# Kernel optimization log

Measured on AMD Instinct MI355X. Metric: run time of the kernel, lower is better.

Reference implementation:

```python
import jax, jax.numpy as jnp
import numpy as np

B, N, C = 4, 2048, 768
H = 12
DH = C // H
HID = 4 * C
EPS = 1e-5


def layer_norm(x, g, b):
    mu = jnp.mean(x, axis=-1, keepdims=True)
    var = jnp.mean(jnp.square(x - mu), axis=-1, keepdims=True)
    return (x - mu) * jax.lax.rsqrt(var + EPS) * g + b


def setup_inputs() -> dict:
    key = jax.random.key(0)
    ks = jax.random.split(key, 8)
    s = 0.02
    return {
        "x": jax.random.normal(ks[0], (B, N, C), dtype=jnp.float32),
        "ln1_g": jnp.ones((C,), jnp.float32),
        "ln1_b": jnp.zeros((C,), jnp.float32),
        # weights stored [in, out] (transpose of torch Linear.weight)
        "w_qkv": jax.random.normal(ks[1], (C, 3 * C), jnp.float32) * s,
        "w_proj": jax.random.normal(ks[2], (C, C), jnp.float32) * s,
        "b_proj": jnp.zeros((C,), jnp.float32),
        "ln2_g": jnp.ones((C,), jnp.float32),
        "ln2_b": jnp.zeros((C,), jnp.float32),
        "w1": jax.random.normal(ks[3], (C, HID), jnp.float32) * s,
        "b1": jnp.zeros((HID,), jnp.float32),
        "w2": jax.random.normal(ks[4], (HID, C), jnp.float32) * s,
        "b2": jnp.zeros((C,), jnp.float32),
    }


def reference(x, ln1_g, ln1_b, w_qkv, w_proj, b_proj, ln2_g, ln2_b, w1, b1, w2, b2):
    # --- attention sub-block (qkv_bias=False, eval mode: dropout/droppath = identity) ---
    h = layer_norm(x, ln1_g, ln1_b)
    qkv = (h @ w_qkv).reshape(B, N, 3, H, DH)          # [B,N,3,H,Dh]
    q, k, v = (qkv[:, :, i].transpose(0, 2, 1, 3) for i in range(3))  # [B,H,N,Dh]
    scale = DH ** -0.5
    attn = jax.nn.softmax(jnp.einsum("bhnd,bhmd->bhnm", q, k) * scale, axis=-1)
    o = jnp.einsum("bhnm,bhmd->bhnd", attn, v).transpose(0, 2, 1, 3).reshape(B, N, C)
    x = x + (o @ w_proj + b_proj)
    # --- MLP sub-block (exact GELU, matching torch nn.GELU) ---
    h2 = layer_norm(x, ln2_g, ln2_b)
    m = jax.nn.gelu(h2 @ w1 + b1, approximate=False) @ w2 + b2
    return x + m
```

## Files before the change

kernel.cpp:

```cpp
#include <hip/hip_runtime.h>
#include <hip/hip_bf16.h>

#define B_ 4
#define N_ 2048
#define C_ 768
#define H_ 12
#define DH_ 64
#define HID_ 3072
#define ROWS_ (B_*N_)

typedef short short8 __attribute__((ext_vector_type(8)));
typedef float f32x4 __attribute__((ext_vector_type(4)));

static __device__ __forceinline__ unsigned short f2bf(float f) {
    __hip_bfloat16 h = __float2bfloat16(f);
    unsigned short u;
    __builtin_memcpy(&u, &h, 2);
    return u;
}

static __device__ __forceinline__ void gload16(const unsigned short* g, unsigned short* l) {
    __builtin_amdgcn_global_load_lds(
        (const __attribute__((address_space(1))) unsigned int*)g,
        (__attribute__((address_space(3))) unsigned int*)l, 16, 0, 0);
}

__global__ __launch_bounds__(256, 4) void ln_kernel(
    const float* __restrict__ x, const float* __restrict__ g,
    const float* __restrict__ bta, unsigned short* __restrict__ out) {
    int row = blockIdx.x;
    const float* xr = x + (size_t)row * C_;
    int t = threadIdx.x;
    float v0 = xr[t], v1 = xr[t + 256], v2 = xr[t + 512];
    float s = v0 + v1 + v2, ss = v0*v0 + v1*v1 + v2*v2;
    #pragma unroll
    for (int o = 32; o > 0; o >>= 1) { s += __shfl_down(s, o); ss += __shfl_down(ss, o); }
    __shared__ float red[10];
    int wid = t >> 6;
    if ((t & 63) == 0) { red[wid] = s; red[4 + wid] = ss; }
    __syncthreads();
    if (t == 0) {
        float S = red[0] + red[1] + red[2] + red[3];
        float SS = red[4] + red[5] + red[6] + red[7];
        float mu = S * (1.0f / C_);
        float var = SS * (1.0f / C_) - mu * mu;
        red[8] = mu; red[9] = rsqrtf(var + 1e-5f);
    }
    __syncthreads();
    float mu = red[8], rs = red[9];
    unsigned short* orow = out + (size_t)row * C_;
    orow[t]       = f2bf((v0 - mu) * rs * g[t]       + bta[t]);
    orow[t + 256] = f2bf((v1 - mu) * rs * g[t + 256] + bta[t + 256]);
    orow[t + 512] = f2bf((v2 - mu) * rs * g[t + 512] + bta[t + 512]);
}

__global__ __launch_bounds__(256, 4) void convT_kernel(
    const float* __restrict__ in, unsigned short* __restrict__ out, int K, int NN) {
    __shared__ float tile[32][33];
    int n0 = blockIdx.x * 32, k0 = blockIdx.y * 32;
    int tx = threadIdx.x & 31, ty = threadIdx.x >> 5;
    #pragma unroll
    for (int j = 0; j < 4; j++)
        tile[ty + j*8][tx] = in[(size_t)(k0 + ty + j*8) * NN + n0 + tx];
    __syncthreads();
    #pragma unroll
    for (int j = 0; j < 4; j++)
        out[(size_t)(n0 + ty + j*8) * K + k0 + tx] = f2bf(tile[tx][ty + j*8]);
}

template<int EPI>
__global__ __launch_bounds__(256, 2) void gemm_kernel(
    const unsigned short* __restrict__ A, const unsigned short* __restrict__ Bt,
    int K, int NN,
    const float* __restrict__ bias, const float* __restrict__ res,
    void* __restrict__ outp,
    unsigned short* __restrict__ qo, unsigned short* __restrict__ ko,
    unsigned short* __restrict__ vto) {
    __shared__ unsigned short Al[128 * 64];
    __shared__ unsigned short Bl[128 * 64];
    const int t = threadIdx.x;
    const int rowA0 = blockIdx.y * 128;
    const int colB0 = blockIdx.x * 128;
    const int wave = t >> 6, lane = t & 63;
    const int wm = wave >> 1, wn = wave & 1;
    const int lr = lane & 15, lg = lane >> 4;

    f32x4 acc[4][4];
    #pragma unroll
    for (int m = 0; m < 4; m++)
        #pragma unroll
        for (int n = 0; n < 4; n++)
            acc[m][n] = (f32x4){0.f, 0.f, 0.f, 0.f};

    const int srow = wave * 32 + (lane >> 3);
    const int scol = (lane & 7) * 8;
    const unsigned short* Ag = A  + (size_t)(rowA0 + srow) * K + scol;
    const unsigned short* Bg = Bt + (size_t)(colB0 + srow) * K + scol;

    for (int kt = 0; kt < K; kt += 64) {
        __syncthreads();
        #pragma unroll
        for (int j = 0; j < 4; j++) {
            gload16(Ag + (size_t)j * 8 * K + kt, Al + (wave * 32 + j * 8) * 64);
            gload16(Bg + (size_t)j * 8 * K + kt, Bl + (wave * 32 + j * 8) * 64);
        }
        __syncthreads();
        #pragma unroll
        for (int kk = 0; kk < 2; kk++) {
            short8 af[4], bf[4];
            #pragma unroll
            for (int m = 0; m < 4; m++)
                af[m] = *(const short8*)(Al + (wm*64 + m*16 + lr) * 64 + kk*32 + lg*8);
            #pragma unroll
            for (int n = 0; n < 4; n++)
                bf[n] = *(const short8*)(Bl + (wn*64 + n*16 + lr) * 64 + kk*32 + lg*8);
            #pragma unroll
            for (int m = 0; m < 4; m++)
                #pragma unroll
                for (int n = 0; n < 4; n++)
                    acc[m][n] = __builtin_amdgcn_mfma_f32_16x16x32_bf16(af[m], bf[n], acc[m][n], 0, 0, 0);
        }
    }
    #pragma unroll
    for (int m = 0; m < 4; m++) {
        #pragma unroll
        for (int n = 0; n < 4; n++) {
            int gc = colB0 + wn*64 + n*16 + lr;
            #pragma unroll
            for (int r2 = 0; r2 < 4; r2++) {
                int gr = rowA0 + wm*64 + m*16 + lg*4 + r2;
                float val = acc[m][n][r2];
                if (EPI == 0) {
                    int which = gc / C_;
                    int cc = gc - which * C_;
                    int hh = cc >> 6, d = cc & 63;
                    int bb = gr >> 11, nn2 = gr & 2047;
                    size_t bh = (size_t)bb * H_ + hh;
                    if (which == 0)      qo[(bh * N_ + nn2) * DH_ + d] = f2bf(val * 0.125f);
                    else if (which == 1) ko[(bh * N_ + nn2) * DH_ + d] = f2bf(val);
                    else                 vto[(bh * DH_ + d) * N_ + nn2] = f2bf(val);
                } else if (EPI == 1) {
                    size_t idx = (size_t)gr * NN + gc;
                    ((float*)outp)[idx] = res[idx] + val + bias[gc];
                } else {
                    float xg = val + bias[gc];
                    float gl = 0.5f * xg * (1.0f + erff(xg * 0.7071067811865476f));
                    ((unsigned short*)outp)[(size_t)gr * NN + gc] = f2bf(gl);
                }
            }
        }
    }
}

__global__ __launch_bounds__(256, 2) void attn_kernel(
    const unsigned short* __restrict__ q, const unsigned short* __restrict__ k,
    const unsigned short* __restrict__ vt, unsigned short* __restrict__ o) {
    __shared__ unsigned short Kl[64 * 64];
    __shared__ unsigned short Vl[64 * 64];
    __shared__ unsigned short Pl[4][16 * 72];
    const int qt = blockIdx.x;
    const int bh = blockIdx.y;
    const int b = bh / H_, h = bh - b * H_;
    const size_t base = (size_t)bh * N_ * DH_;
    const int t = threadIdx.x, wave = t >> 6, lane = t & 63;
    const int lr = lane & 15, lg = lane >> 4;

    const int qrow = qt * 64 + wave * 16 + lr;
    short8 qf[2];
    #pragma unroll
    for (int ks = 0; ks < 2; ks++)
        qf[ks] = *(const short8*)(q + base + (size_t)qrow * DH_ + ks * 32 + lg * 8);

    f32x4 oacc[4];
    #pragma unroll
    for (int d = 0; d < 4; d++) oacc[d] = (f32x4){0.f, 0.f, 0.f, 0.f};
    float mi[4] = {-1e30f, -1e30f, -1e30f, -1e30f};
    float li[4] = {0.f, 0.f, 0.f, 0.f};

    for (int kt2 = 0; kt2 < N_ / 64; kt2++) {
        __syncthreads();
        #pragma unroll
        for (int half = 0; half < 2; half++) {
            int cid = t + half * 256;
            int r = cid >> 3, cc = cid & 7;
            int sw = (cc * 16) ^ ((r & 7) << 4);
            short8 vk = *(const short8*)(k + base + (size_t)(kt2 * 64 + r) * DH_ + cc * 8);
            *(short8*)((char*)Kl + r * 128 + sw) = vk;
            short8 vv = *(const short8*)(vt + base + (size_t)r * N_ + kt2 * 64 + cc * 8);
            *(short8*)((char*)Vl + r * 128 + sw) = vv;
        }
        __syncthreads();
        f32x4 s[4];
        #pragma unroll
        for (int cb = 0; cb < 4; cb++) {
            s[cb] = (f32x4){0.f, 0.f, 0.f, 0.f};
            #pragma unroll
            for (int ks = 0; ks < 2; ks++) {
                int key = cb * 16 + lr;
                int bytecol = ks * 64 + lg * 16;
                short8 kf = *(const short8*)((char*)Kl + key * 128 + (bytecol ^ ((key & 7) << 4)));
                s[cb] = __builtin_amdgcn_mfma_f32_16x16x32_bf16(qf[ks], kf, s[cb], 0, 0, 0);
            }
        }
        float al[4], rs[4];
        #pragma unroll
        for (int i = 0; i < 4; i++) {
            float mx = fmaxf(fmaxf(s[0][i], s[1][i]), fmaxf(s[2][i], s[3][i]));
            #pragma unroll
            for (int off = 1; off < 16; off <<= 1) mx = fmaxf(mx, __shfl_xor(mx, off));
            float mn = fmaxf(mi[i], mx);
            al[i] = __expf(mi[i] - mn);
            mi[i] = mn;
            rs[i] = 0.f;
        }
        #pragma unroll
        for (int cb = 0; cb < 4; cb++)
            #pragma unroll
            for (int i = 0; i < 4; i++) {
                float p = __expf(s[cb][i] - mi[i]);
                s[cb][i] = p;
                rs[i] += p;
            }
        #pragma unroll
        for (int i = 0; i < 4; i++) {
            #pragma unroll
            for (int off = 1; off < 16; off <<= 1) rs[i] += __shfl_xor(rs[i], off);
            li[i] = li[i] * al[i] + rs[i];
        }
        #pragma unroll
        for (int d = 0; d < 4; d++) {
            f32x4 tmp = oacc[d];
            tmp[0] *= al[0]; tmp[1] *= al[1]; tmp[2] *= al[2]; tmp[3] *= al[3];
            oacc[d] = tmp;
        }
        unsigned short* pw = Pl[wave];
        #pragma unroll
        for (int cb = 0; cb < 4; cb++)
            #pragma unroll
            for (int i = 0; i < 4; i++)
                pw[(lg * 4 + i) * 72 + cb * 16 + lr] = f2bf(s[cb][i]);
        __syncthreads();
        #pragma unroll
        for (int ks = 0; ks < 2; ks++) {
            short8 pf = *(const short8*)(pw + lr * 72 + ks * 32 + lg * 8);
            #pragma unroll
            for (int db = 0; db < 4; db++) {
                int dh = db * 16 + lr;
                int bytecol = ks * 64 + lg * 16;
                short8 vf = *(const short8*)((char*)Vl + dh * 128 + (bytecol ^ ((dh & 7) << 4)));
                oacc[db] = __builtin_amdgcn_mfma_f32_16x16x32_bf16(pf, vf, oacc[db], 0, 0, 0);
            }
        }
    }
    #pragma unroll
    for (int db = 0; db < 4; db++)
        #pragma unroll
        for (int i = 0; i < 4; i++) {
            int row = qt * 64 + wave * 16 + lg * 4 + i;
            int col = h * 64 + db * 16 + lr;
            o[((size_t)b * N_ + row) * C_ + col] = f2bf(oacc[db][i] / li[i]);
        }
}

extern "C" void kernel_launch(void* const* d_in, const int* in_sizes, int n_in,
                              void* d_out, int out_size, void* d_ws, size_t ws_size,
                              hipStream_t stream) {
    (void)in_sizes; (void)n_in; (void)out_size; (void)ws_size;
    const float* x      = (const float*)d_in[0];
    const float* ln1_g  = (const float*)d_in[1];
    const float* ln1_b  = (const float*)d_in[2];
    const float* w_qkv  = (const float*)d_in[3];
    const float* w_proj = (const float*)d_in[4];
    const float* b_proj = (const float*)d_in[5];
    const float* ln2_g  = (const float*)d_in[6];
    const float* ln2_b  = (const float*)d_in[7];
    const float* w1     = (const float*)d_in[8];
    const float* b1     = (const float*)d_in[9];
    const float* w2     = (const float*)d_in[10];
    const float* b2     = (const float*)d_in[11];
    float* out = (float*)d_out;

    char* ws = (char*)d_ws;
    size_t off = 0;
    auto alloc = [&](size_t bytes) {
        char* p = ws + off;
        off += (bytes + 255) & ~(size_t)255;
        return p;
    };
    unsigned short* hb     = (unsigned short*)alloc((size_t)ROWS_ * C_ * 2);
    unsigned short* wqkvT  = (unsigned short*)alloc((size_t)C_ * 3 * C_ * 2);
    unsigned short* wprojT = (unsigned short*)alloc((size_t)C_ * C_ * 2);
    unsigned short* w1T    = (unsigned short*)alloc((size_t)C_ * HID_ * 2);
    unsigned short* w2T    = (unsigned short*)alloc((size_t)HID_ * C_ * 2);
    unsigned short* uni    = (unsigned short*)alloc((size_t)ROWS_ * HID_ * 2);
    unsigned short* qb  = uni;
    unsigned short* kb  = qb  + (size_t)B_ * H_ * N_ * DH_;
    unsigned short* vtb = kb  + (size_t)B_ * H_ * N_ * DH_;
    unsigned short* ob  = vtb + (size_t)B_ * H_ * N_ * DH_;
    unsigned short* mid = uni;

    convT_kernel<<<dim3(3 * C_ / 32, C_ / 32), 256, 0, stream>>>(w_qkv, wqkvT, C_, 3 * C_);
    convT_kernel<<<dim3(C_ / 32, C_ / 32), 256, 0, stream>>>(w_proj, wprojT, C_, C_);
    convT_kernel<<<dim3(HID_ / 32, C_ / 32), 256, 0, stream>>>(w1, w1T, C_, HID_);
    convT_kernel<<<dim3(C_ / 32, HID_ / 32), 256, 0, stream>>>(w2, w2T, HID_, C_);

    ln_kernel<<<ROWS_, 256, 0, stream>>>(x, ln1_g, ln1_b, hb);
    gemm_kernel<0><<<dim3(3 * C_ / 128, ROWS_ / 128), 256, 0, stream>>>(
        hb, wqkvT, C_, 3 * C_, nullptr, nullptr, nullptr, qb, kb, vtb);
    attn_kernel<<<dim3(N_ / 64, B_ * H_), 256, 0, stream>>>(qb, kb, vtb, ob);
    gemm_kernel<1><<<dim3(C_ / 128, ROWS_ / 128), 256, 0, stream>>>(
        ob, wprojT, C_, C_, b_proj, x, (void*)out, nullptr, nullptr, nullptr);
    ln_kernel<<<ROWS_, 256, 0, stream>>>(out, ln2_g, ln2_b, hb);
    gemm_kernel<2><<<dim3(HID_ / 128, ROWS_ / 128), 256, 0, stream>>>(
        hb, w1T, C_, HID_, b1, nullptr, (void*)mid, nullptr, nullptr, nullptr);
    gemm_kernel<1><<<dim3(C_ / 128, ROWS_ / 128), 256, 0, stream>>>(
        mid, w2T, HID_, C_, b2, out, (void*)out, nullptr, nullptr, nullptr);
}
```

Measured before the change: 528.3 us.

## Double query rows per attention wave, prefetch K/V into registers, skip rescaling

The attention kernel now has each wave process 32 query rows (128 per block), so every K fragment read from shared memory is reused across two row groups. The next K/V tile is loaded into registers while the current one is being computed, and the old mid-loop barrier is removed. Softmax now uses exp2 with log2(e) folded into the Q scale, and it skips the rescale of the running max when no row's max grows. The cost is higher register pressure and only half as many blocks in the grid, which may reduce occupancy.

After: 517.8 us. -2.0%, faster.

```diff
diff --git a/kernel.cpp b/kernel.cpp
--- a/kernel.cpp
+++ b/kernel.cpp
@@ -136,7 +136,7 @@
                     int hh = cc >> 6, d = cc & 63;
                     int bb = gr >> 11, nn2 = gr & 2047;
                     size_t bh = (size_t)bb * H_ + hh;
-                    if (which == 0)      qo[(bh * N_ + nn2) * DH_ + d] = f2bf(val * 0.125f);
+                    if (which == 0)      qo[(bh * N_ + nn2) * DH_ + d] = f2bf(val * 0.1803368801f);
                     else if (which == 1) ko[(bh * N_ + nn2) * DH_ + d] = f2bf(val);
                     else                 vto[(bh * DH_ + d) * N_ + nn2] = f2bf(val);
                 } else if (EPI == 1) {
@@ -165,101 +165,139 @@
     const int t = threadIdx.x, wave = t >> 6, lane = t & 63;
     const int lr = lane & 15, lg = lane >> 4;
 
-    const int qrow = qt * 64 + wave * 16 + lr;
-    short8 qf[2];
-    #pragma unroll
-    for (int ks = 0; ks < 2; ks++)
-        qf[ks] = *(const short8*)(q + base + (size_t)qrow * DH_ + ks * 32 + lg * 8);
-
-    f32x4 oacc[4];
-    #pragma unroll
-    for (int d = 0; d < 4; d++) oacc[d] = (f32x4){0.f, 0.f, 0.f, 0.f};
-    float mi[4] = {-1e30f, -1e30f, -1e30f, -1e30f};
-    float li[4] = {0.f, 0.f, 0.f, 0.f};
-
-    for (int kt2 = 0; kt2 < N_ / 64; kt2++) {
+    short8 qf[2][2];
+    #pragma unroll
+    for (int ro = 0; ro < 2; ro++) {
+        int qrow = qt * 128 + wave * 32 + ro * 16 + lr;
+        #pragma unroll
+        for (int ks = 0; ks < 2; ks++)
+            qf[ro][ks] = *(const short8*)(q + base + (size_t)qrow * DH_ + ks * 32 + lg * 8);
+    }
+
+    f32x4 oacc[2][4];
+    float mi[2][4], li[2][4];
+    #pragma unroll
+    for (int ro = 0; ro < 2; ro++) {
+        #pragma unroll
+        for (int d = 0; d < 4; d++) oacc[ro][d] = (f32x4){0.f, 0.f, 0.f, 0.f};
+        #pragma unroll
+        for (int i = 0; i < 4; i++) { mi[ro][i] = -1e30f; li[ro][i] = 0.f; }
+    }
+
+    const int sr0 = t >> 3, sr1 = sr0 + 32, scc = t & 7;
+    const unsigned short* kg0 = k  + base + (size_t)sr0 * DH_ + scc * 8;
+    const unsigned short* kg1 = k  + base + (size_t)sr1 * DH_ + scc * 8;
+    const unsigned short* vg0 = vt + base + (size_t)sr0 * N_  + scc * 8;
+    const unsigned short* vg1 = vt + base + (size_t)sr1 * N_  + scc * 8;
+    const int sw0 = (scc * 16) ^ ((sr0 & 7) << 4);
+    const int sw1 = (scc * 16) ^ ((sr1 & 7) << 4);
+
+    short8 kreg0 = *(const short8*)kg0, kreg1 = *(const short8*)kg1;
+    short8 vreg0 = *(const short8*)vg0, vreg1 = *(const short8*)vg1;
+
+    const int NT = N_ / 64;
+    for (int kt2 = 0; kt2 < NT; kt2++) {
         __syncthreads();
-        #pragma unroll
-        for (int half = 0; half < 2; half++) {
-            int cid = t + half * 256;
-            int r = cid >> 3, cc = cid & 7;
-            int sw = (cc * 16) ^ ((r & 7) << 4);
-            short8 vk = *(const short8*)(k + base + (size_t)(kt2 * 64 + r) * DH_ + cc * 8);
-            *(short8*)((char*)Kl + r * 128 + sw) = vk;
-            short8 vv = *(const short8*)(vt + base + (size_t)r * N_ + kt2 * 64 + cc * 8);
-            *(short8*)((char*)Vl + r * 128 + sw) = vv;
-        }
+        *(short8*)((char*)Kl + sr0 * 128 + sw0) = kreg0;
+        *(short8*)((char*)Kl + sr1 * 128 + sw1) = kreg1;
+        *(short8*)((char*)Vl + sr0 * 128 + sw0) = vreg0;
+        *(short8*)((char*)Vl + sr1 * 128 + sw1) = vreg1;
         __syncthreads();
-        f32x4 s[4];
+        if (kt2 + 1 < NT) {
+            kreg0 = *(const short8*)(kg0 + (size_t)(kt2 + 1) * 64 * DH_);
+            kreg1 = *(const short8*)(kg1 + (size_t)(kt2 + 1) * 64 * DH_);
+            vreg0 = *(const short8*)(vg0 + (size_t)(kt2 + 1) * 64);
+            vreg1 = *(const short8*)(vg1 + (size_t)(kt2 + 1) * 64);
+        }
+        short8 kf[4][2];
         #pragma unroll
         for (int cb = 0; cb < 4; cb++) {
-            s[cb] = (f32x4){0.f, 0.f, 0.f, 0.f};
+            int key = cb * 16 + lr;
             #pragma unroll
             for (int ks = 0; ks < 2; ks++) {
-                int key = cb * 16 + lr;
                 int bytecol = ks * 64 + lg * 16;
-                short8 kf = *(const short8*)((char*)Kl + key * 128 + (bytecol ^ ((key & 7) << 4)));
-                s[cb] = __builtin_amdgcn_mfma_f32_16x16x32_bf16(qf[ks], kf, s[cb], 0, 0, 0);
-            }
-        }
-        float al[4], rs[4];
-        #pragma unroll
-        for (int i = 0; i < 4; i++) {
-            float mx = fmaxf(fmaxf(s[0][i], s[1][i]), fmaxf(s[2][i], s[3][i]));
-            #pragma unroll
-            for (int off = 1; off < 16; off <<= 1) mx = fmaxf(mx, __shfl_xor(mx, off));
-            float mn = fmaxf(mi[i], mx);
-            al[i] = __expf(mi[i] - mn);
-            mi[i] = mn;
-            rs[i] = 0.f;
-        }
-        #pragma unroll
-        for (int cb = 0; cb < 4; cb++)
+                kf[cb][ks] = *(const short8*)((char*)Kl + key * 128 + (bytecol ^ ((key & 7) << 4)));
+            }
+        }
+        unsigned short* pw = Pl[wave];
+        #pragma unroll
+        for (int ro = 0; ro < 2; ro++) {
+            f32x4 s[4];
+            #pragma unroll
+            for (int cb = 0; cb < 4; cb++) {
+                s[cb] = (f32x4){0.f, 0.f, 0.f, 0.f};
+                #pragma unroll
+                for (int ks = 0; ks < 2; ks++)
+                    s[cb] = __builtin_amdgcn_mfma_f32_16x16x32_bf16(qf[ro][ks], kf[cb][ks], s[cb], 0, 0, 0);
+            }
+            float mx[4];
             #pragma unroll
             for (int i = 0; i < 4; i++) {
-                float p = __expf(s[cb][i] - mi[i]);
-                s[cb][i] = p;
-                rs[i] += p;
-            }
-        #pragma unroll
-        for (int i = 0; i < 4; i++) {
-            #pragma unroll
-            for (int off = 1; off < 16; off <<= 1) rs[i] += __shfl_xor(rs[i], off);
-            li[i] = li[i] * al[i] + rs[i];
-        }
-        #pragma unroll
-        for (int d = 0; d < 4; d++) {
-            f32x4 tmp = oacc[d];
-            tmp[0] *= al[0]; tmp[1] *= al[1]; tmp[2] *= al[2]; tmp[3] *= al[3];
-            oacc[d] = tmp;
-        }
-        unsigned short* pw = Pl[wave];
-        #pragma unroll
-        for (int cb = 0; cb < 4; cb++)
-            #pragma unroll
-            for (int i = 0; i < 4; i++)
-                pw[(lg * 4 + i) * 72 + cb * 16 + lr] = f2bf(s[cb][i]);
-        __syncthreads();
-        #pragma unroll
-        for (int ks = 0; ks < 2; ks++) {
-            short8 pf = *(const short8*)(pw + lr * 72 + ks * 32 + lg * 8);
-            #pragma unroll
-            for (int db = 0; db < 4; db++) {
-                int dh = db * 16 + lr;
-                int bytecol = ks * 64 + lg * 16;
-                short8 vf = *(const short8*)((char*)Vl + dh * 128 + (bytecol ^ ((dh & 7) << 4)));
-                oacc[db] = __builtin_amdgcn_mfma_f32_16x16x32_bf16(pf, vf, oacc[db], 0, 0, 0);
-            }
-        }
-    }
-    #pragma unroll
-    for (int db = 0; db < 4; db++)
-        #pragma unroll
-        for (int i = 0; i < 4; i++) {
-            int row = qt * 64 + wave * 16 + lg * 4 + i;
-            int col = h * 64 + db * 16 + lr;
-            o[((size_t)b * N_ + row) * C_ + col] = f2bf(oacc[db][i] / li[i]);
-        }
+                float m0 = fmaxf(fmaxf(s[0][i], s[1][i]), fmaxf(s[2][i], s[3][i]));
+                #pragma unroll
+                for (int off = 1; off < 16; off <<= 1) m0 = fmaxf(m0, __shfl_xor(m0, off));
+                mx[i] = m0;
+            }
+            int gf = 0;
+            #pragma unroll
+            for (int i = 0; i < 4; i++) gf |= (mx[i] > mi[ro][i]) ? 1 : 0;
+            if (__any(gf)) {
+                #pragma unroll
+                for (int i = 0; i < 4; i++) {
+                    float mn = fmaxf(mi[ro][i], mx[i]);
+                    float al = exp2f(mi[ro][i] - mn);
+                    mi[ro][i] = mn;
+                    li[ro][i] *= al;
+                    #pragma unroll
+                    for (int db = 0; db < 4; db++) oacc[ro][db][i] *= al;
+                }
+            }
+            float rs[4] = {0.f, 0.f, 0.f, 0.f};
+            #pragma unroll
+            for (int cb = 0; cb < 4; cb++)
+                #pragma unroll
+                for (int i = 0; i < 4; i++) {
+                    float p = exp2f(s[cb][i] - mi[ro][i]);
+                    s[cb][i] = p;
+                    rs[i] += p;
+                }
+            #pragma unroll
+            for (int i = 0; i < 4; i++) {
+                #pragma unroll
+                for (int off = 1; off < 16; off <<= 1) rs[i] += __shfl_xor(rs[i], off);
+                li[ro][i] += rs[i];
+            }
+            #pragma unroll
+            for (int cb = 0; cb < 4; cb++)
+                #pragma unroll
+                for (int i = 0; i < 4; i++)
+                    pw[(lg * 4 + i) * 72 + cb * 16 + lr] = f2bf(s[cb][i]);
+            short8 pf[2];
+            #pragma unroll
+            for (int ks = 0; ks < 2; ks++)
+                pf[ks] = *(const short8*)(pw + lr * 72 + ks * 32 + lg * 8);
+            #pragma unroll
+            for (int ks = 0; ks < 2; ks++) {
+                #pragma unroll
+                for (int db = 0; db < 4; db++) {
+                    int dh = db * 16 + lr;
+                    int bytecol = ks * 64 + lg * 16;
+                    short8 vf = *(const short8*)((char*)Vl + dh * 128 + (bytecol ^ ((dh & 7) << 4)));
+                    oacc[ro][db] = __builtin_amdgcn_mfma_f32_16x16x32_bf16(pf[ks], vf, oacc[ro][db], 0, 0, 0);
+                }
+            }
+        }
+    }
+    #pragma unroll
+    for (int ro = 0; ro < 2; ro++)
+        #pragma unroll
+        for (int db = 0; db < 4; db++)
+            #pragma unroll
+            for (int i = 0; i < 4; i++) {
+                int row = qt * 128 + wave * 32 + ro * 16 + lg * 4 + i;
+                int col = h * 64 + db * 16 + lr;
+                o[((size_t)b * N_ + row) * C_ + col] = f2bf(oacc[ro][db][i] / li[ro][i]);
+            }
 }
 
 extern "C" void kernel_launch(void* const* d_in, const int* in_sizes, int n_in,
@@ -307,7 +345,7 @@
     ln_kernel<<<ROWS_, 256, 0, stream>>>(x, ln1_g, ln1_b, hb);
     gemm_kernel<0><<<dim3(3 * C_ / 128, ROWS_ / 128), 256, 0, stream>>>(
         hb, wqkvT, C_, 3 * C_, nullptr, nullptr, nullptr, qb, kb, vtb);
-    attn_kernel<<<dim3(N_ / 64, B_ * H_), 256, 0, stream>>>(qb, kb, vtb, ob);
+    attn_kernel<<<dim3(N_ / 128, B_ * H_), 256, 0, stream>>>(qb, kb, vtb, ob);
     gemm_kernel<1><<<dim3(C_ / 128, ROWS_ / 128), 256, 0, stream>>>(
         ob, wprojT, C_, C_, b_proj, x, (void*)out, nullptr, nullptr, nullptr);
     ln_kernel<<<ROWS_, 256, 0, stream>>>(out, ln2_g, ln2_b, hb);
```

## Restructure attention to transposed S and keep P in registers

Applied to the files above, without the earlier changes.

The attention kernel now computes S transposed (K as the A operand), so each lane owns one query row. The P tile stays in registers as the PV operand, which removes the shared-memory round trip and the third barrier. K/V loads are register-prefetched one tile ahead, the log2e factor is folded into the Q scale so exp2f can be used, output rescaling is skipped when no row max changes, and launch bounds rise to 4 blocks per CU. The risks are register pressure at the higher occupancy target and the overhead of the wave-uniform branch.

New measurement: 461.1 us. -12.7%, faster.

```diff
diff --git a/kernel.cpp b/kernel.cpp
--- a/kernel.cpp
+++ b/kernel.cpp
@@ -10,6 +10,8 @@
 #define ROWS_ (B_*N_)
 
 typedef short short8 __attribute__((ext_vector_type(8)));
+typedef short short4v __attribute__((ext_vector_type(4)));
+typedef unsigned short ushort4v __attribute__((ext_vector_type(4)));
 typedef float f32x4 __attribute__((ext_vector_type(4)));
 
 static __device__ __forceinline__ unsigned short f2bf(float f) {
@@ -136,7 +138,7 @@
                     int hh = cc >> 6, d = cc & 63;
                     int bb = gr >> 11, nn2 = gr & 2047;
                     size_t bh = (size_t)bb * H_ + hh;
-                    if (which == 0)      qo[(bh * N_ + nn2) * DH_ + d] = f2bf(val * 0.125f);
+                    if (which == 0)      qo[(bh * N_ + nn2) * DH_ + d] = f2bf(val * 0.1803368801f);
                     else if (which == 1) ko[(bh * N_ + nn2) * DH_ + d] = f2bf(val);
                     else                 vto[(bh * DH_ + d) * N_ + nn2] = f2bf(val);
                 } else if (EPI == 1) {
@@ -152,12 +154,11 @@
     }
 }
 
-__global__ __launch_bounds__(256, 2) void attn_kernel(
+__global__ __launch_bounds__(256, 4) void attn_kernel(
     const unsigned short* __restrict__ q, const unsigned short* __restrict__ k,
     const unsigned short* __restrict__ vt, unsigned short* __restrict__ o) {
     __shared__ unsigned short Kl[64 * 64];
     __shared__ unsigned short Vl[64 * 64];
-    __shared__ unsigned short Pl[4][16 * 72];
     const int qt = blockIdx.x;
     const int bh = blockIdx.y;
     const int b = bh / H_, h = bh - b * H_;
@@ -171,95 +172,104 @@
     for (int ks = 0; ks < 2; ks++)
         qf[ks] = *(const short8*)(q + base + (size_t)qrow * DH_ + ks * 32 + lg * 8);
 
-    f32x4 oacc[4];
-    #pragma unroll
-    for (int d = 0; d < 4; d++) oacc[d] = (f32x4){0.f, 0.f, 0.f, 0.f};
-    float mi[4] = {-1e30f, -1e30f, -1e30f, -1e30f};
-    float li[4] = {0.f, 0.f, 0.f, 0.f};
-
-    for (int kt2 = 0; kt2 < N_ / 64; kt2++) {
+    f32x4 oaccT[4];
+    #pragma unroll
+    for (int d = 0; d < 4; d++) oaccT[d] = (f32x4){0.f, 0.f, 0.f, 0.f};
+    float mi = -1e30f, li = 0.f;
+
+    const int sr0 = t >> 3, sr1 = sr0 + 32, scc = t & 7;
+    const unsigned short* kg0 = k  + base + (size_t)sr0 * DH_ + scc * 8;
+    const unsigned short* kg1 = k  + base + (size_t)sr1 * DH_ + scc * 8;
+    const unsigned short* vg0 = vt + base + (size_t)sr0 * N_  + scc * 8;
+    const unsigned short* vg1 = vt + base + (size_t)sr1 * N_  + scc * 8;
+    const int sw0 = (scc * 16) ^ ((sr0 & 7) << 4);
+    const int sw1 = (scc * 16) ^ ((sr1 & 7) << 4);
+
+    short8 kreg0 = *(const short8*)kg0, kreg1 = *(const short8*)kg1;
+    short8 vreg0 = *(const short8*)vg0, vreg1 = *(const short8*)vg1;
+
+    const int NT = N_ / 64;
+    for (int kt2 = 0; kt2 < NT; kt2++) {
         __syncthreads();
-        #pragma unroll
-        for (int half = 0; half < 2; half++) {
-            int cid = t + half * 256;
-            int r = cid >> 3, cc = cid & 7;
-            int sw = (cc * 16) ^ ((r & 7) << 4);
-            short8 vk = *(const short8*)(k + base + (size_t)(kt2 * 64 + r) * DH_ + cc * 8);
-            *(short8*)((char*)Kl + r * 128 + sw) = vk;
-            short8 vv = *(const short8*)(vt + base + (size_t)r * N_ + kt2 * 64 + cc * 8);
-            *(short8*)((char*)Vl + r * 128 + sw) = vv;
-        }
+        *(short8*)((char*)Kl + sr0 * 128 + sw0) = kreg0;
+        *(short8*)((char*)Kl + sr1 * 128 + sw1) = kreg1;
+        *(short8*)((char*)Vl + sr0 * 128 + sw0) = vreg0;
+        *(short8*)((char*)Vl + sr1 * 128 + sw1) = vreg1;
         __syncthreads();
+        if (kt2 + 1 < NT) {
+            kreg0 = *(const short8*)(kg0 + (size_t)(kt2 + 1) * 64 * DH_);
+            kreg1 = *(const short8*)(kg1 + (size_t)(kt2 + 1) * 64 * DH_);
+            vreg0 = *(const short8*)(vg0 + (size_t)(kt2 + 1) * 64);
+            vreg1 = *(const short8*)(vg1 + (size_t)(kt2 + 1) * 64);
+        }
         f32x4 s[4];
         #pragma unroll
         for (int cb = 0; cb < 4; cb++) {
             s[cb] = (f32x4){0.f, 0.f, 0.f, 0.f};
+            int key = cb * 16 + lr;
             #pragma unroll
             for (int ks = 0; ks < 2; ks++) {
-                int key = cb * 16 + lr;
                 int bytecol = ks * 64 + lg * 16;
                 short8 kf = *(const short8*)((char*)Kl + key * 128 + (bytecol ^ ((key & 7) << 4)));
-                s[cb] = __builtin_amdgcn_mfma_f32_16x16x32_bf16(qf[ks], kf, s[cb], 0, 0, 0);
-            }
-        }
-        float al[4], rs[4];
-        #pragma unroll
-        for (int i = 0; i < 4; i++) {
-            float mx = fmaxf(fmaxf(s[0][i], s[1][i]), fmaxf(s[2][i], s[3][i]));
-            #pragma unroll
-            for (int off = 1; off < 16; off <<= 1) mx = fmaxf(mx, __shfl_xor(mx, off));
-            float mn = fmaxf(mi[i], mx);
-            al[i] = __expf(mi[i] - mn);
-            mi[i] = mn;
-            rs[i] = 0.f;
-        }
+                s[cb] = __builtin_amdgcn_mfma_f32_16x16x32_bf16(kf, qf[ks], s[cb], 0, 0, 0);
+            }
+        }
+        float mx = fmaxf(fmaxf(fmaxf(s[0][0], s[0][1]), fmaxf(s[0][2], s[0][3])),
+                         fmaxf(fmaxf(s[1][0], s[1][1]), fmaxf(s[1][2], s[1][3])));
+        mx = fmaxf(mx, fmaxf(fmaxf(fmaxf(s[2][0], s[2][1]), fmaxf(s[2][2], s[2][3])),
+                             fmaxf(fmaxf(s[3][0], s[3][1]), fmaxf(s[3][2], s[3][3]))));
+        mx = fmaxf(mx, __shfl_xor(mx, 16));
+        mx = fmaxf(mx, __shfl_xor(mx, 32));
+        if (__any(mx > mi)) {
+            float mn = fmaxf(mi, mx);
+            float al = exp2f(mi - mn);
+            mi = mn;
+            li *= al;
+            #pragma unroll
+            for (int db = 0; db < 4; db++) oaccT[db] *= al;
+        }
+        float rs = 0.f;
         #pragma unroll
         for (int cb = 0; cb < 4; cb++)
             #pragma unroll
             for (int i = 0; i < 4; i++) {
-                float p = __expf(s[cb][i] - mi[i]);
+                float p = exp2f(s[cb][i] - mi);
                 s[cb][i] = p;
-                rs[i] += p;
-            }
-        #pragma unroll
-        for (int i = 0; i < 4; i++) {
-            #pragma unroll
-            for (int off = 1; off < 16; off <<= 1) rs[i] += __shfl_xor(rs[i], off);
-            li[i] = li[i] * al[i] + rs[i];
-        }
-        #pragma unroll
-        for (int d = 0; d < 4; d++) {
-            f32x4 tmp = oacc[d];
-            tmp[0] *= al[0]; tmp[1] *= al[1]; tmp[2] *= al[2]; tmp[3] *= al[3];
-            oacc[d] = tmp;
-        }
-        unsigned short* pw = Pl[wave];
-        #pragma unroll
-        for (int cb = 0; cb < 4; cb++)
-            #pragma unroll
-            for (int i = 0; i < 4; i++)
-                pw[(lg * 4 + i) * 72 + cb * 16 + lr] = f2bf(s[cb][i]);
-        __syncthreads();
+                rs += p;
+            }
+        rs += __shfl_xor(rs, 16);
+        rs += __shfl_xor(rs, 32);
+        li += rs;
         #pragma unroll
         for (int ks = 0; ks < 2; ks++) {
-            short8 pf = *(const short8*)(pw + lr * 72 + ks * 32 + lg * 8);
+            short8 pb;
+            #pragma unroll
+            for (int i = 0; i < 4; i++) {
+                pb[i]     = (short)f2bf(s[2*ks][i]);
+                pb[i + 4] = (short)f2bf(s[2*ks + 1][i]);
+            }
             #pragma unroll
             for (int db = 0; db < 4; db++) {
                 int dh = db * 16 + lr;
-                int bytecol = ks * 64 + lg * 16;
-                short8 vf = *(const short8*)((char*)Vl + dh * 128 + (bytecol ^ ((dh & 7) << 4)));
-                oacc[db] = __builtin_amdgcn_mfma_f32_16x16x32_bf16(pf, vf, oacc[db], 0, 0, 0);
-            }
-        }
-    }
-    #pragma unroll
-    for (int db = 0; db < 4; db++)
-        #pragma unroll
-        for (int i = 0; i < 4; i++) {
-            int row = qt * 64 + wave * 16 + lg * 4 + i;
-            int col = h * 64 + db * 16 + lr;
-            o[((size_t)b * N_ + row) * C_ + col] = f2bf(oacc[db][i] / li[i]);
-        }
+                int swz = (dh & 7) << 4;
+                short4v v0 = *(const short4v*)((char*)Vl + dh * 128 + ((ks * 64 + lg * 8) ^ swz));
+                short4v v1 = *(const short4v*)((char*)Vl + dh * 128 + ((ks * 64 + 32 + lg * 8) ^ swz));
+                short8 vf;
+                #pragma unroll
+                for (int i = 0; i < 4; i++) { vf[i] = v0[i]; vf[i + 4] = v1[i]; }
+                oaccT[db] = __builtin_amdgcn_mfma_f32_16x16x32_bf16(vf, pb, oaccT[db], 0, 0, 0);
+            }
+        }
+    }
+    float inv = 1.0f / li;
+    unsigned short* orow = o + ((size_t)b * N_ + qrow) * C_ + h * 64;
+    #pragma unroll
+    for (int db = 0; db < 4; db++) {
+        ushort4v pk;
+        #pragma unroll
+        for (int i = 0; i < 4; i++) pk[i] = f2bf(oaccT[db][i] * inv);
+        *(ushort4v*)(orow + db * 16 + lg * 4) = pk;
+    }
 }
 
 extern "C" void kernel_launch(void* const* d_in, const int* in_sizes, int n_in,
```
